# Performance work log

Measured on AMD Instinct MI355X. Metric: run time of the kernel, lower is better.

The kernel has to match this reference:

```python
import jax, jax.numpy as jnp
import numpy as np

EPS_NORM = 1e-12   # F.normalize eps
EPS_Q = 1e-5       # quant scale clamp

def simple_rmsnorm(x):
    # F.normalize(x, dim=-1) * sqrt(dim)  ==  x / sqrt(mean(x^2))
    d = x.shape[-1]
    n = jnp.maximum(jnp.linalg.norm(x, axis=-1, keepdims=True), EPS_NORM)
    return x / n * jnp.sqrt(jnp.asarray(d, x.dtype))

def activation_quant(x):
    # per-token 8-bit absmax quant
    scale = 127.0 / jnp.clip(jnp.max(jnp.abs(x), axis=-1, keepdims=True), EPS_Q, None)
    return jnp.clip(jnp.round(x * scale), -128.0, 127.0) / scale

def weight_quant(w):
    # per-tensor ternary quant: scale = 1 / mean|w|
    scale = 1.0 / jnp.clip(jnp.mean(jnp.abs(w)), EPS_Q, None)
    return jnp.clip(jnp.round(w * scale), -1.0, 1.0) / scale

def bitlinear158(x, w):
    xn = simple_rmsnorm(x)
    # straight-through estimators
    xq = xn + jax.lax.stop_gradient(activation_quant(xn) - xn)
    wq = w + jax.lax.stop_gradient(weight_quant(w) - w)
    # w is [out, in] like nn.Linear
    return jnp.einsum('bsd,od->bso', xq, wq)

def setup_inputs() -> dict:
    key = jax.random.key(0)
    k1, k2, k3 = jax.random.split(key, 3)
    dim, inner = 2048, 8192
    x = jax.random.normal(k1, (4, 2048, dim), dtype=jnp.float32)
    w1 = jax.random.normal(k2, (inner, dim), dtype=jnp.float32) * 0.02
    w2 = jax.random.normal(k3, (dim, inner), dtype=jnp.float32) * 0.02
    return {"x": x, "w1": w1, "w2": w2}

def reference(x, w1, w2):
    h = bitlinear158(x, w1)
    h = jax.nn.gelu(h, approximate=False)  # nn.GELU() default = exact erf
    return bitlinear158(h, w2)
```

## Files before the change

### kernel.cpp

```cpp
#include <hip/hip_runtime.h>
#include <hip/hip_bf16.h>
#include <hip/hip_fp16.h>

typedef __attribute__((ext_vector_type(4))) int i32x4;
typedef __attribute__((ext_vector_type(8))) unsigned short u16x8;
typedef __attribute__((ext_vector_type(8))) char c8;
typedef __attribute__((ext_vector_type(4))) char c4;
typedef unsigned int u32;
typedef unsigned short u16;

#define SCH0() __builtin_amdgcn_sched_barrier(0)

__device__ __forceinline__ void gload_lds16(const void* g, void* l) {
  __builtin_amdgcn_global_load_lds((const u32 __attribute__((address_space(1)))*)g,
                                   (u32 __attribute__((address_space(3)))*)l, 16, 0, 0);
}
__device__ __forceinline__ float h2f(u16 u) { return __half2float(__ushort_as_half(u)); }
__device__ __forceinline__ u16  f2h(float f){ return __half_as_ushort(__float2half_rn(f)); }

__global__ __launch_bounds__(256) void prep_kernel(const float* __restrict__ x,
    char* __restrict__ qx, float* __restrict__ invs,
    const float* __restrict__ w1, const float* __restrict__ w2,
    double* __restrict__ part) {
  const int tid = threadIdx.x;
  __shared__ double sd[256];
  __shared__ float sf[256];
  if (blockIdx.x < 8192) {
    const int D = 2048;
    int row = blockIdx.x;
    const float* xr = x + (size_t)row * D;
    float4 a = ((const float4*)xr)[tid * 2], b = ((const float4*)xr)[tid * 2 + 1];
    float v[8] = {a.x, a.y, a.z, a.w, b.x, b.y, b.z, b.w};
    double ss = 0; float mx = 0.0f;
#pragma unroll
    for (int i = 0; i < 8; i++) { ss += (double)v[i] * v[i]; mx = fmaxf(mx, fabsf(v[i])); }
    sd[tid] = ss; sf[tid] = mx; __syncthreads();
    for (int o = 128; o > 0; o >>= 1) {
      if (tid < o) { sd[tid] += sd[tid + o]; sf[tid] = fmaxf(sf[tid], sf[tid + o]); }
      __syncthreads();
    }
    __shared__ float bn, bs;
    if (tid == 0) {
      float n = fmaxf((float)sqrt(sd[0]), 1e-12f);
      float amax = sf[0] * (sqrtf((float)D) / n);
      float cl = fmaxf(amax, 1e-5f);
      bn = n; bs = 127.0f / cl;
      invs[row] = cl / 127.0f;
    }
    __syncthreads();
    float n = bn, s = bs, sq = sqrtf((float)D);
    c8 q;
#pragma unroll
    for (int i = 0; i < 8; i++) {
      float xn = (v[i] / n) * sq;
      float r = rintf(xn * s);
      r = fminf(fmaxf(r, -128.0f), 127.0f);
      q[i] = (char)(int)r;
    }
    *(c8*)&qx[(size_t)row * D + tid * 8] = q;
  } else {
    const int n4 = 4194304;
    const bool isw2 = blockIdx.x >= 8704;
    const float* w = isw2 ? w2 : w1;
    const int vb = blockIdx.x - (isw2 ? 8704 : 8192);
    double s = 0;
    for (int i = vb * 256 + tid; i < n4; i += 512 * 256) {
      float4 v = ((const float4*)w)[i];
      s += (double)fabsf(v.x) + (double)fabsf(v.y) + (double)fabsf(v.z) + (double)fabsf(v.w);
    }
    sd[tid] = s; __syncthreads();
    for (int o = 128; o > 0; o >>= 1) { if (tid < o) sd[tid] += sd[tid + o]; __syncthreads(); }
    if (tid == 0) part[(isw2 ? 512 : 0) + vb] = sd[0];
  }
}

__global__ __launch_bounds__(256) void wscale_final(const double* __restrict__ part,
    float* __restrict__ wsc) {
  int tid = threadIdx.x;
  __shared__ double sd[256];
  sd[tid] = part[tid] + part[tid + 256]; __syncthreads();
  for (int o = 128; o > 0; o >>= 1) { if (tid < o) sd[tid] += sd[tid + o]; __syncthreads(); }
  double s1 = sd[0]; __syncthreads();
  sd[tid] = part[512 + tid] + part[768 + tid]; __syncthreads();
  for (int o = 128; o > 0; o >>= 1) { if (tid < o) sd[tid] += sd[tid + o]; __syncthreads(); }
  if (tid == 0) {
    float m1 = (float)(s1 / 16777216.0);
    float m2 = (float)(sd[0] / 16777216.0);
    float d1 = fmaxf(m1, 1e-5f), d2 = fmaxf(m2, 1e-5f);
    wsc[0] = 1.0f / d1; wsc[1] = d1; wsc[2] = 1.0f / d2; wsc[3] = d2;
  }
}

__global__ __launch_bounds__(256) void quant_w_kernel(const float* __restrict__ w1,
    char* __restrict__ q1, const float* __restrict__ w2, char* __restrict__ q2,
    const float* __restrict__ wsc) {
  const int n4 = 4194304;
  const bool isw2 = blockIdx.x >= 2048;
  const float* w = isw2 ? w2 : w1;
  char* q = isw2 ? q2 : q1;
  float s = isw2 ? wsc[2] : wsc[0];
  const int vb = blockIdx.x - (isw2 ? 2048 : 0);
  for (int i = vb * 256 + threadIdx.x; i < n4; i += 2048 * 256) {
    float4 v = ((const float4*)w)[i];
    c4 o;
    o[0] = (char)(int)(fminf(fmaxf(rintf(v.x * s), -1.0f), 1.0f));
    o[1] = (char)(int)(fminf(fmaxf(rintf(v.y * s), -1.0f), 1.0f));
    o[2] = (char)(int)(fminf(fmaxf(rintf(v.z * s), -1.0f), 1.0f));
    o[3] = (char)(int)(fminf(fmaxf(rintf(v.w * s), -1.0f), 1.0f));
    ((c4*)q)[i] = o;
  }
}

#define READ_A3(BUF, HALF, DST)                                            \
  { _Pragma("unroll") for (int f_ = 0; f_ < 4; f_++)                       \
      DST[f_] = *(const i32x4*)&sm[BUF][0][(wm * 128 + (HALF) * 64 + llo + f_ * 16) * 64 + koff]; }
#define READ_B3(BUF, HALF, DST)                                            \
  { _Pragma("unroll") for (int f_ = 0; f_ < 2; f_++)                       \
      DST[f_] = *(const i32x4*)&sm[BUF][1][(wn * 64 + (HALF) * 32 + llo + f_ * 16) * 64 + koff]; }
#define MMAQ(AV, BV, MH, NH)                                               \
  { _Pragma("unroll") for (int m_ = 0; m_ < 4; m_++)                       \
      _Pragma("unroll") for (int n_ = 0; n_ < 2; n_++)                     \
        acc[(MH) * 4 + m_][(NH) * 2 + n_] =                                \
            __builtin_amdgcn_mfma_i32_16x16x64_i8(AV[m_], BV[n_],          \
                acc[(MH) * 4 + m_][(NH) * 2 + n_], 0, 0, 0); }
#define STAGE3(BUF, KT)                                                    \
  { size_t ko_ = (size_t)(KT) * 64;                                        \
    gload_lds16(gA0 + ko_, &sm[BUF][0][tid * 16]);                         \
    gload_lds16(gB0 + ko_, &sm[BUF][1][tid * 16]);                         \
    gload_lds16(gA1 + ko_, &sm[BUF][0][8192 + tid * 16]);                  \
    gload_lds16(gB1 + ko_, &sm[BUF][1][8192 + tid * 16]); }
#define TILE_M(BR, BN, BS, KT)                                             \
  { STAGE3(BS, (KT) + 2);                                                  \
    SCH0();                                                                \
    READ_B3(BR, 1, bhi); SCH0();                                           \
    MMAQ(alo, blo, 0, 0); SCH0();                                          \
    READ_A3(BR, 1, ahi); SCH0();                                           \
    MMAQ(alo, bhi, 0, 1);                                                  \
    MMAQ(ahi, blo, 1, 0); SCH0();                                          \
    asm volatile("s_waitcnt vmcnt(4) lgkmcnt(0)\n\ts_barrier" ::: "memory"); \
    READ_A3(BN, 0, alo); READ_B3(BN, 0, blo); SCH0();                      \
    MMAQ(ahi, bhi, 1, 1); }

template <int EPI>
__global__ __launch_bounds__(512, 2) void gemm_i8(const char* __restrict__ A,
    const char* __restrict__ B, int N, int K, size_t ldA, size_t ldB, int gridN,
    const float* __restrict__ rowscale, const float* __restrict__ wsc,
    int widx, void* __restrict__ outp) {
  __shared__ __align__(16) char sm[3][2][16384];
  const int tid = threadIdx.x;
  const int lane = tid & 63, w = tid >> 6;
  const int wm = w >> 2, wn = w & 3;
  const int llo = lane & 15, lhi = lane >> 4;
  const int koff = ((lhi ^ ((llo >> 1) & 3)) << 4);

  const int nwg = gridDim.x, cpx = nwg >> 3;
  const int swz = (blockIdx.x & 7) * cpx + (blockIdx.x >> 3);
  const int band = gridN << 2;
  const int g = swz / band, idx = swz % band;
  const int bm = (g << 2) + (idx & 3), bn = idx >> 2;

  const int NT = K >> 6;
  const int NITER = (NT - 2) / 3;

  const int rs = tid >> 2;
  const int kbs = (((tid & 3) ^ ((tid >> 3) & 3)) << 4);
  const char* gA0 = A + (size_t)(bm * 256 + rs) * ldA + kbs;
  const char* gA1 = gA0 + (size_t)128 * ldA;
  const char* gB0 = B + (size_t)(bn * 256 + rs) * ldB + kbs;
  const char* gB1 = gB0 + (size_t)128 * ldB;

  i32x4 alo[4], ahi[4], blo[2], bhi[2];
  i32x4 acc[8][4];
#pragma unroll
  for (int m = 0; m < 8; m++)
#pragma unroll
    for (int n = 0; n < 4; n++) acc[m][n] = (i32x4){0, 0, 0, 0};

  STAGE3(0, 0);
  asm volatile("s_nop 0" ::: "memory");
  STAGE3(1, 1);
  asm volatile("s_waitcnt vmcnt(4)\n\ts_barrier" ::: "memory");
  READ_A3(0, 0, alo); READ_B3(0, 0, blo);

  for (int it = 0, t = 0; it < NITER; ++it, t += 3) {
    TILE_M(0, 1, 2, t);
    TILE_M(1, 2, 0, t + 1);
    TILE_M(2, 0, 1, t + 2);
  }
  {
    SCH0();
    READ_B3(0, 1, bhi); SCH0();
    MMAQ(alo, blo, 0, 0); SCH0();
    READ_A3(0, 1, ahi); SCH0();
    MMAQ(alo, bhi, 0, 1);
    MMAQ(ahi, blo, 1, 0); SCH0();
    asm volatile("s_waitcnt vmcnt(0) lgkmcnt(0)\n\ts_barrier" ::: "memory");
    READ_A3(1, 0, alo); READ_B3(1, 0, blo); SCH0();
    MMAQ(ahi, bhi, 1, 1);
  }
  {
    READ_B3(1, 1, bhi);
    MMAQ(alo, blo, 0, 0);
    READ_A3(1, 1, ahi);
    MMAQ(alo, bhi, 0, 1);
    MMAQ(ahi, blo, 1, 0);
    MMAQ(ahi, bhi, 1, 1);
  }

  float wdeq = wsc[widx];
#pragma unroll
  for (int mf = 0; mf < 8; mf++) {
#pragma unroll
    for (int reg = 0; reg < 4; reg++) {
      int r = bm * 256 + wm * 128 + mf * 16 + lhi * 4 + reg;
      float deq = rowscale[r] * wdeq;
#pragma unroll
      for (int nf = 0; nf < 4; nf++) {
        int c = bn * 256 + wn * 64 + nf * 16 + llo;
        float val = (float)acc[mf][nf][reg] * deq;
        if (EPI == 0) {
          float gg = 0.5f * val * (1.0f + erff(val * 0.70710678118654752440f));
          ((u16*)outp)[(size_t)r * N + c] = f2h(gg);
        } else {
          ((float*)outp)[(size_t)r * N + c] = val;
        }
      }
    }
  }
}

__global__ __launch_bounds__(256) void quant_h_kernel(u16* __restrict__ h, float* __restrict__ invs) {
  const int D = 8192;
  int row = blockIdx.x, tid = threadIdx.x;
  u16* hr = h + (size_t)row * D;
  float v[32];
#pragma unroll
  for (int j = 0; j < 4; j++) {
    u16x8 u = *(const u16x8*)&hr[j * 2048 + tid * 8];
#pragma unroll
    for (int e = 0; e < 8; e++) v[j * 8 + e] = h2f(u[e]);
  }
  double ss = 0; float mx = 0.0f;
#pragma unroll
  for (int i = 0; i < 32; i++) { ss += (double)v[i] * v[i]; mx = fmaxf(mx, fabsf(v[i])); }
  __shared__ double sd[256]; __shared__ float sf[256];
  sd[tid] = ss; sf[tid] = mx; __syncthreads();
  for (int o = 128; o > 0; o >>= 1) {
    if (tid < o) { sd[tid] += sd[tid + o]; sf[tid] = fmaxf(sf[tid], sf[tid + o]); }
    __syncthreads();
  }
  __shared__ float bn, bs;
  if (tid == 0) {
    float n = fmaxf((float)sqrt(sd[0]), 1e-12f);
    float amax = sf[0] * (sqrtf((float)D) / n);
    float cl = fmaxf(amax, 1e-5f);
    bn = n; bs = 127.0f / cl;
    invs[row] = cl / 127.0f;
  }
  __syncthreads();
  float n = bn, s = bs, sq = sqrtf((float)D);
  char* hq = (char*)hr;
#pragma unroll
  for (int j = 0; j < 4; j++) {
    c8 q;
#pragma unroll
    for (int e = 0; e < 8; e++) {
      float xn = (v[j * 8 + e] / n) * sq;
      float r = rintf(xn * s);
      r = fminf(fmaxf(r, -128.0f), 127.0f);
      q[e] = (char)(int)r;
    }
    *(c8*)&hq[j * 2048 + tid * 8] = q;
  }
}

extern "C" void kernel_launch(void* const* d_in, const int* in_sizes, int n_in,
                              void* d_out, int out_size, void* d_ws, size_t ws_size,
                              hipStream_t stream) {
  const float* x  = (const float*)d_in[0];
  const float* w1 = (const float*)d_in[1];
  const float* w2 = (const float*)d_in[2];

  char* ws = (char*)d_ws;
  char*   qx     = (char*)(ws + 0);
  char*   w1q    = (char*)(ws + 16777216);
  char*   w2q    = (char*)(ws + 33554432);
  u16*    h      = (u16*)(ws + 50331648);
  float*  invs_x = (float*)(ws + 184549376);
  float*  invs_h = (float*)(ws + 184582144);
  double* part   = (double*)(ws + 184614912);
  float*  wsc    = (float*)(ws + 184623104);

  prep_kernel<<<9216, 256, 0, stream>>>(x, qx, invs_x, w1, w2, part);
  wscale_final<<<1, 256, 0, stream>>>(part, wsc);
  quant_w_kernel<<<4096, 256, 0, stream>>>(w1, w1q, w2, w2q, wsc);
  gemm_i8<0><<<1024, 512, 0, stream>>>(qx, w1q, 8192, 2048, 2048, 2048, 32,
                                       invs_x, wsc, 1, (void*)h);
  quant_h_kernel<<<8192, 256, 0, stream>>>(h, invs_h);
  gemm_i8<1><<<256, 512, 0, stream>>>((const char*)h, w2q, 2048, 8192, 16384, 8192, 8,
                                      invs_h, wsc, 3, d_out);
}
```

Baseline: 423.4 us.

## Use 16 waves per GEMM block with 64x64 per-wave tiles

Moves the int8 GEMM from 8 waves per 256x256 tile (128x64 per wave) to 16 waves (1024 threads, 64x64 per wave). Each thread issues one global-to-LDS load per operand per k-step, and the split lo/hi interleaved schedule becomes a single read-then-16-MFMA step per tile. The aim is more waves to hide latency and fewer accumulator registers per thread. In exchange, the LDS-read to MFMA ratio rises and the software interleaving of reads with MFMAs is lost. Launch bounds of (1024,4) may also be unachievable given the LDS size.

After: 406.5 us, median of 3. 4.0% less time.

```diff
diff --git a/kernel.cpp b/kernel.cpp
--- a/kernel.cpp
+++ b/kernel.cpp
@@ -111,38 +111,31 @@
   }
 }
 
-#define READ_A3(BUF, HALF, DST)                                            \
+#define READ_A4(BUF)                                                       \
   { _Pragma("unroll") for (int f_ = 0; f_ < 4; f_++)                       \
-      DST[f_] = *(const i32x4*)&sm[BUF][0][(wm * 128 + (HALF) * 64 + llo + f_ * 16) * 64 + koff]; }
-#define READ_B3(BUF, HALF, DST)                                            \
-  { _Pragma("unroll") for (int f_ = 0; f_ < 2; f_++)                       \
-      DST[f_] = *(const i32x4*)&sm[BUF][1][(wn * 64 + (HALF) * 32 + llo + f_ * 16) * 64 + koff]; }
-#define MMAQ(AV, BV, MH, NH)                                               \
+      a[f_] = *(const i32x4*)&sm[BUF][0][(wm * 64 + f_ * 16 + llo) * 64 + koff]; }
+#define READ_B4(BUF)                                                       \
+  { _Pragma("unroll") for (int f_ = 0; f_ < 4; f_++)                       \
+      b[f_] = *(const i32x4*)&sm[BUF][1][(wn * 64 + f_ * 16 + llo) * 64 + koff]; }
+#define MMAQ16()                                                           \
   { _Pragma("unroll") for (int m_ = 0; m_ < 4; m_++)                       \
-      _Pragma("unroll") for (int n_ = 0; n_ < 2; n_++)                     \
-        acc[(MH) * 4 + m_][(NH) * 2 + n_] =                                \
-            __builtin_amdgcn_mfma_i32_16x16x64_i8(AV[m_], BV[n_],          \
-                acc[(MH) * 4 + m_][(NH) * 2 + n_], 0, 0, 0); }
-#define STAGE3(BUF, KT)                                                    \
+      _Pragma("unroll") for (int n_ = 0; n_ < 4; n_++)                     \
+        acc[m_][n_] = __builtin_amdgcn_mfma_i32_16x16x64_i8(a[m_], b[n_],  \
+                                                            acc[m_][n_], 0, 0, 0); }
+#define STAGE4(BUF, KT)                                                    \
   { size_t ko_ = (size_t)(KT) * 64;                                        \
-    gload_lds16(gA0 + ko_, &sm[BUF][0][tid * 16]);                         \
-    gload_lds16(gB0 + ko_, &sm[BUF][1][tid * 16]);                         \
-    gload_lds16(gA1 + ko_, &sm[BUF][0][8192 + tid * 16]);                  \
-    gload_lds16(gB1 + ko_, &sm[BUF][1][8192 + tid * 16]); }
-#define TILE_M(BR, BN, BS, KT)                                             \
-  { STAGE3(BS, (KT) + 2);                                                  \
+    gload_lds16(gA + ko_, &sm[BUF][0][tid * 16]);                          \
+    gload_lds16(gB + ko_, &sm[BUF][1][tid * 16]); }
+#define TILE4(BR, BS, KT)                                                  \
+  { STAGE4(BS, (KT) + 2);                                                  \
     SCH0();                                                                \
-    READ_B3(BR, 1, bhi); SCH0();                                           \
-    MMAQ(alo, blo, 0, 0); SCH0();                                          \
-    READ_A3(BR, 1, ahi); SCH0();                                           \
-    MMAQ(alo, bhi, 0, 1);                                                  \
-    MMAQ(ahi, blo, 1, 0); SCH0();                                          \
-    asm volatile("s_waitcnt vmcnt(4) lgkmcnt(0)\n\ts_barrier" ::: "memory"); \
-    READ_A3(BN, 0, alo); READ_B3(BN, 0, blo); SCH0();                      \
-    MMAQ(ahi, bhi, 1, 1); }
+    READ_A4(BR); READ_B4(BR);                                              \
+    MMAQ16();                                                              \
+    SCH0();                                                                \
+    asm volatile("s_waitcnt vmcnt(2) lgkmcnt(0)\n\ts_barrier" ::: "memory"); }
 
 template <int EPI>
-__global__ __launch_bounds__(512, 2) void gemm_i8(const char* __restrict__ A,
+__global__ __launch_bounds__(1024, 4) void gemm_i8(const char* __restrict__ A,
     const char* __restrict__ B, int N, int K, size_t ldA, size_t ldB, int gridN,
     const float* __restrict__ rowscale, const float* __restrict__ wsc,
     int widx, void* __restrict__ outp) {
@@ -164,55 +157,43 @@
 
   const int rs = tid >> 2;
   const int kbs = (((tid & 3) ^ ((tid >> 3) & 3)) << 4);
-  const char* gA0 = A + (size_t)(bm * 256 + rs) * ldA + kbs;
-  const char* gA1 = gA0 + (size_t)128 * ldA;
-  const char* gB0 = B + (size_t)(bn * 256 + rs) * ldB + kbs;
-  const char* gB1 = gB0 + (size_t)128 * ldB;
-
-  i32x4 alo[4], ahi[4], blo[2], bhi[2];
-  i32x4 acc[8][4];
-#pragma unroll
-  for (int m = 0; m < 8; m++)
+  const char* gA = A + (size_t)(bm * 256 + rs) * ldA + kbs;
+  const char* gB = B + (size_t)(bn * 256 + rs) * ldB + kbs;
+
+  i32x4 a[4], b[4];
+  i32x4 acc[4][4];
+#pragma unroll
+  for (int m = 0; m < 4; m++)
 #pragma unroll
     for (int n = 0; n < 4; n++) acc[m][n] = (i32x4){0, 0, 0, 0};
 
-  STAGE3(0, 0);
+  STAGE4(0, 0);
   asm volatile("s_nop 0" ::: "memory");
-  STAGE3(1, 1);
-  asm volatile("s_waitcnt vmcnt(4)\n\ts_barrier" ::: "memory");
-  READ_A3(0, 0, alo); READ_B3(0, 0, blo);
+  STAGE4(1, 1);
+  asm volatile("s_waitcnt vmcnt(2)\n\ts_barrier" ::: "memory");
 
   for (int it = 0, t = 0; it < NITER; ++it, t += 3) {
-    TILE_M(0, 1, 2, t);
-    TILE_M(1, 2, 0, t + 1);
-    TILE_M(2, 0, 1, t + 2);
+    TILE4(0, 2, t);
+    TILE4(1, 0, t + 1);
+    TILE4(2, 1, t + 2);
   }
   {
+    READ_A4(0); READ_B4(0);
+    MMAQ16();
     SCH0();
-    READ_B3(0, 1, bhi); SCH0();
-    MMAQ(alo, blo, 0, 0); SCH0();
-    READ_A3(0, 1, ahi); SCH0();
-    MMAQ(alo, bhi, 0, 1);
-    MMAQ(ahi, blo, 1, 0); SCH0();
     asm volatile("s_waitcnt vmcnt(0) lgkmcnt(0)\n\ts_barrier" ::: "memory");
-    READ_A3(1, 0, alo); READ_B3(1, 0, blo); SCH0();
-    MMAQ(ahi, bhi, 1, 1);
   }
   {
-    READ_B3(1, 1, bhi);
-    MMAQ(alo, blo, 0, 0);
-    READ_A3(1, 1, ahi);
-    MMAQ(alo, bhi, 0, 1);
-    MMAQ(ahi, blo, 1, 0);
-    MMAQ(ahi, bhi, 1, 1);
+    READ_A4(1); READ_B4(1);
+    MMAQ16();
   }
 
   float wdeq = wsc[widx];
 #pragma unroll
-  for (int mf = 0; mf < 8; mf++) {
+  for (int mf = 0; mf < 4; mf++) {
 #pragma unroll
     for (int reg = 0; reg < 4; reg++) {
-      int r = bm * 256 + wm * 128 + mf * 16 + lhi * 4 + reg;
+      int r = bm * 256 + wm * 64 + mf * 16 + lhi * 4 + reg;
       float deq = rowscale[r] * wdeq;
 #pragma unroll
       for (int nf = 0; nf < 4; nf++) {
@@ -294,9 +275,9 @@
   prep_kernel<<<9216, 256, 0, stream>>>(x, qx, invs_x, w1, w2, part);
   wscale_final<<<1, 256, 0, stream>>>(part, wsc);
   quant_w_kernel<<<4096, 256, 0, stream>>>(w1, w1q, w2, w2q, wsc);
-  gemm_i8<0><<<1024, 512, 0, stream>>>(qx, w1q, 8192, 2048, 2048, 2048, 32,
-                                       invs_x, wsc, 1, (void*)h);
+  gemm_i8<0><<<1024, 1024, 0, stream>>>(qx, w1q, 8192, 2048, 2048, 2048, 32,
+                                        invs_x, wsc, 1, (void*)h);
   quant_h_kernel<<<8192, 256, 0, stream>>>(h, invs_h);
-  gemm_i8<1><<<256, 512, 0, stream>>>((const char*)h, w2q, 2048, 8192, 16384, 8192, 8,
-                                      invs_h, wsc, 3, d_out);
-}
+  gemm_i8<1><<<256, 1024, 0, stream>>>((const char*)h, w2q, 2048, 8192, 16384, 8192, 8,
+                                       invs_h, wsc, 3, d_out);
+}
```
